# Kernel optimization log

Measured on AMD Instinct MI355X. Metric: run time of the kernel, lower is better.

The kernel has to match this reference:

```python
import jax, jax.numpy as jnp
import numpy as np

EPS = 1.1920929e-07  # torch.finfo(float32).eps
TOP_K = 2
AUX_COEF = 0.01

def rmsnorm(x):
    return x * jax.lax.rsqrt(jnp.mean(x * x, axis=-1, keepdims=True) + EPS)

def setup_inputs() -> dict:
    key = jax.random.key(0)
    ks = jax.random.split(key, 8)
    B, T, C, H, E = 1, 2048, 1024, 2048, 8
    x = jax.random.normal(ks[0], (B, T, C), jnp.float32)
    gate_w = jax.random.normal(ks[1], (E, C), jnp.float32) * 0.02
    w1 = jax.random.normal(ks[2], (E, H, C), jnp.float32) * 0.02  # expert up-proj
    w2 = jax.random.normal(ks[3], (E, C, H), jnp.float32) * 0.02  # expert down-proj
    shared_gate_w = jax.random.normal(ks[4], (1, C), jnp.float32) * 0.02
    k_w = jax.random.normal(ks[5], (H, C), jnp.float32) * 0.02
    k_b = jax.random.normal(ks[6], (H,), jnp.float32) * 0.01
    v_w = jax.random.normal(ks[7], (C, H), jnp.float32) * 0.02
    v_b = jnp.zeros((C,), jnp.float32)
    return dict(x=x, gate_w=gate_w, w1=w1, w2=w2, shared_gate_w=shared_gate_w,
                k_w=k_w, k_b=k_b, v_w=v_w, v_b=v_b)

def reference(x, gate_w, w1, w2, shared_gate_w, k_w, k_b, v_w, v_b):
    B, T, C = x.shape
    xt = rmsnorm(x.reshape(-1, C))                     # [N,C]
    N = xt.shape[0]
    raw = xt @ gate_w.T                                # [N,E]
    scores = jax.nn.softmax(raw, axis=-1)
    topk_w, topk_idx = jax.lax.top_k(scores, TOP_K)    # [N,k]
    topk_w = topk_w / (jnp.sum(topk_w, axis=-1, keepdims=True) + 1e-6)
    E = scores.shape[-1]
    rows = jnp.arange(N)[:, None]
    onehot = jnp.zeros_like(scores).at[rows, topk_idx].set(1.0 / TOP_K)
    aux_loss = E * jnp.sum(jnp.mean(onehot, 0) * jnp.mean(scores, 0)) * AUX_COEF
    # dense gate matrix [N,E]: combine weight per (token, expert)
    g = jnp.zeros_like(scores).at[rows, topk_idx].add(topk_w)
    # grouped-GEMM expressed densely over experts (reference math identical)
    h = jnp.einsum('nc,ehc->neh', xt, w1)              # [N,E,H]
    h = jnp.square(jax.nn.relu(h)) * g[:, :, None]     # act + gate-combine weight
    out = jnp.einsum('neh,ech->nc', h, w2)             # [N,C]
    # shared expert: sigmoid gate * MLP (MLP re-norms its input)
    sg = jax.nn.sigmoid(xt @ shared_gate_w.T)          # [N,1]
    xs = rmsnorm(xt)
    kk = jnp.square(jax.nn.relu(xs @ k_w.T + k_b))     # [N,H]
    shared = kk @ v_w.T + v_b                          # [N,C]
    out = out + sg * shared
    return out.reshape(B, T, C), aux_loss
```

## Files before the change

kernel.cpp:

```cpp
#include <hip/hip_runtime.h>
#include <hip/hip_bf16.h>
#include <stdint.h>

typedef __bf16 bf16;
typedef bf16 bf16x8 __attribute__((ext_vector_type(8)));
typedef bf16 bf16x4 __attribute__((ext_vector_type(4)));
typedef float f32x4 __attribute__((ext_vector_type(4)));

constexpr int N = 2048;
constexpr int C = 1024;
constexpr int H = 2048;
constexpr int E = 8;
constexpr float EPS = 1.1920929e-07f;

constexpr int BM = 128, BN = 256, BK = 32;
constexpr int GT = 32;
constexpr int ATILE = BM * BK * 2;
constexpr int BTILE = BN * BK * 2;

constexpr int PREP_GATE = N / GT;
constexpr int PREP_RMS  = N;
constexpr int CVT_BLK   = ((E * H * C + H * C) / 4) / 1024;
constexpr int PREP_TOTAL = PREP_GATE + PREP_RMS + 2 * CVT_BLK;

constexpr int P1_UP    = E * (N / BM) * (H / BN);
constexpr int P1_KP    = (N / BM) * (H / BN);
constexpr int P1_TOTAL = P1_UP + P1_KP;

constexpr int P2_DOWN  = (E * 2) * (N / BM) * (C / BN);
constexpr int P2_VP    = (N / BM) * (C / BN) * 2;
constexpr int P2_TOTAL = P2_DOWN + P2_VP;

constexpr int COMBINE_BLK = (N * C / 4) / 256;

__device__ __forceinline__ void cvt_pair(const float* __restrict__ s1, bf16* __restrict__ d1,
                                         size_t n1, const float* __restrict__ s2,
                                         bf16* __restrict__ d2, int cbx) {
  size_t base = (size_t)cbx * 1024 + threadIdx.x;
  #pragma unroll
  for (int j = 0; j < 4; ++j) {
    size_t i = base + (size_t)j * 256;
    if (i < n1) {
      float4 v = ((const float4*)s1)[i];
      bf16x4 o = { (bf16)v.x, (bf16)v.y, (bf16)v.z, (bf16)v.w };
      ((bf16x4*)d1)[i] = o;
    } else {
      size_t k = i - n1;
      float4 v = ((const float4*)s2)[k];
      bf16x4 o = { (bf16)v.x, (bf16)v.y, (bf16)v.z, (bf16)v.w };
      ((bf16x4*)d2)[k] = o;
    }
  }
}

__global__ __launch_bounds__(256) void prep_kernel(
    const float* __restrict__ x, const float* __restrict__ gate_w,
    const float* __restrict__ sgw, const float* __restrict__ w1,
    const float* __restrict__ kw, const float* __restrict__ w2,
    const float* __restrict__ vw,
    bf16* __restrict__ xtb, float* __restrict__ rs2_arr,
    float* __restrict__ g, float* __restrict__ sgbuf,
    int* __restrict__ counts, int* __restrict__ lists,
    float* __restrict__ scoresums,
    bf16* __restrict__ w1b, bf16* __restrict__ kwb,
    bf16* __restrict__ w2b, bf16* __restrict__ vwb) {
  __shared__ float s_scores[8];
  __shared__ int   s_cnt[8];
  __shared__ int   s_base[8];
  __shared__ int   s_e1[GT], s_p1[GT], s_e2[GT], s_p2[GT];
  __shared__ float red[4];
  __shared__ float tot;
  const int bx = blockIdx.x;
  const int tid = threadIdx.x, lane = tid & 63, wave = tid >> 6;

  if (bx >= PREP_GATE + PREP_RMS + CVT_BLK) {
    cvt_pair(w2, w2b, (size_t)E * C * H / 4, vw, vwb,
             bx - PREP_GATE - PREP_RMS - CVT_BLK);
    return;
  }
  if (bx >= PREP_GATE + PREP_RMS) {
    cvt_pair(w1, w1b, (size_t)E * H * C / 4, kw, kwb, bx - PREP_GATE - PREP_RMS);
    return;
  }
  if (bx >= PREP_GATE) {
    int n = bx - PREP_GATE;
    float4 v = ((const float4*)(x + (size_t)n * C))[tid];
    float ss = v.x*v.x + v.y*v.y + v.z*v.z + v.w*v.w;
    #pragma unroll
    for (int off = 32; off > 0; off >>= 1) ss += __shfl_down(ss, off, 64);
    if (lane == 0) red[wave] = ss;
    __syncthreads();
    if (tid == 0) tot = red[0] + red[1] + red[2] + red[3];
    __syncthreads();
    float sumsq = tot;
    float rs1 = rsqrtf(sumsq * (1.f / C) + EPS);
    bf16x4 o = { (bf16)(v.x*rs1), (bf16)(v.y*rs1), (bf16)(v.z*rs1), (bf16)(v.w*rs1) };
    ((bf16x4*)(xtb + (size_t)n * C))[tid] = o;
    if (tid == 0) {
      float m2 = sumsq * rs1 * rs1 * (1.f / C);
      rs2_arr[n] = rsqrtf(m2 + EPS);
    }
    return;
  }
  if (tid < 8) { s_scores[tid] = 0.f; s_cnt[tid] = 0; }
  __syncthreads();

  const int tok0 = bx * GT + wave * (GT / 4);
  for (int tt = 0; tt < GT / 4; ++tt) {
    const int tok = tok0 + tt;
    const float* xr = x + (size_t)tok * C;
    float acc[10];
    #pragma unroll
    for (int e = 0; e < 10; e++) acc[e] = 0.f;
    #pragma unroll
    for (int k = 0; k < 16; ++k) {
      int c = k * 64 + lane;
      float xv = xr[c];
      #pragma unroll
      for (int e = 0; e < 8; e++) acc[e] = fmaf(xv, gate_w[e * 1024 + c], acc[e]);
      acc[8] = fmaf(xv, sgw[c], acc[8]);
      acc[9] = fmaf(xv, xv, acc[9]);
    }
    #pragma unroll
    for (int e = 0; e < 10; e++) {
      float v = acc[e];
      #pragma unroll
      for (int off = 32; off > 0; off >>= 1) v += __shfl_xor(v, off, 64);
      acc[e] = v;
    }
    if (lane == 0) {
      float rs1 = rsqrtf(acc[9] * (1.f / C) + EPS);
      float raw[9];
      #pragma unroll
      for (int e = 0; e < 9; e++) raw[e] = acc[e] * rs1;
      float m = raw[0];
      for (int e = 1; e < 8; e++) m = fmaxf(m, raw[e]);
      float sc[8], s = 0.f;
      for (int e = 0; e < 8; e++) { sc[e] = expf(raw[e] - m); s += sc[e]; }
      float inv = 1.f / s;
      for (int e = 0; e < 8; e++) sc[e] *= inv;
      int i1 = 0;
      for (int e = 1; e < 8; e++) if (sc[e] > sc[i1]) i1 = e;
      int i2 = -1;
      for (int e = 0; e < 8; e++) {
        if (e == i1) continue;
        if (i2 < 0 || sc[e] > sc[i2]) i2 = e;
      }
      float denom = sc[i1] + sc[i2] + 1e-6f;
      float* gr = g + (size_t)tok * E;
      #pragma unroll
      for (int e = 0; e < 8; e++) gr[e] = 0.f;
      gr[i1] = sc[i1] / denom;
      gr[i2] = sc[i2] / denom;
      sgbuf[tok] = 1.f / (1.f + expf(-raw[8]));
      for (int e = 0; e < 8; e++) atomicAdd(&s_scores[e], sc[e]);
      int lt = wave * (GT / 4) + tt;
      int p1 = atomicAdd(&s_cnt[i1], 1);
      int p2 = atomicAdd(&s_cnt[i2], 1);
      s_e1[lt] = i1; s_p1[lt] = p1;
      s_e2[lt] = i2; s_p2[lt] = p2;
    }
  }
  __syncthreads();
  if (tid < 8) {
    s_base[tid] = atomicAdd(&counts[tid], s_cnt[tid]);
    atomicAdd(&scoresums[tid], s_scores[tid]);
  }
  __syncthreads();
  if (tid < GT) {
    int tok = bx * GT + tid;
    int e1 = s_e1[tid], e2 = s_e2[tid];
    lists[e1 * N + s_base[e1] + s_p1[tid]] = (tok << 1);
    lists[e2 * N + s_base[e2] + s_p2[tid]] = (tok << 1) | 1;
  }
}

#define GLL(gp, lp)                                                             \
  __builtin_amdgcn_global_load_lds((__attribute__((address_space(1))) void*)(gp), \
                                   (__attribute__((address_space(3))) void*)(lp), 16, 0, 0)

__device__ __forceinline__ void stage_step(
    const char* pA, const char* pB0, const char* pB1,
    char* Ab, char* Bb, int dA, int dB) {
  GLL(pA, Ab + dA);
  GLL(pB0, Bb + dB);
  GLL(pB1, Bb + dB + 1024);
}

__device__ __forceinline__ void mfma_loop(
    const char* pA, const char* pB0, const char* pB1,
    char* As, char* Bs, int dA, int dB, int lane,
    int kIters, int mb, int nb, f32x4 acc[4][4]) {
  const int arow = lane & 15;
  const int koff = (lane >> 4) * 16;
  stage_step(pA, pB0, pB1, As, Bs, dA, dB);
  pA += 64; pB0 += 64; pB1 += 64;
  for (int t = 0; t < kIters; ++t) {
    if (t + 1 < kIters) {
      stage_step(pA, pB0, pB1,
                 As + ((t + 1) & 1) * ATILE, Bs + ((t + 1) & 1) * BTILE, dA, dB);
      pA += 64; pB0 += 64; pB1 += 64;
      asm volatile("s_waitcnt vmcnt(3)" ::: "memory");
    } else {
      asm volatile("s_waitcnt vmcnt(0)" ::: "memory");
    }
    __builtin_amdgcn_s_barrier();
    const char* Ac = As + (t & 1) * ATILE;
    const char* Bc = Bs + (t & 1) * BTILE;
    bf16x8 a[4], b[4];
    #pragma unroll
    for (int i = 0; i < 4; ++i) {
      a[i] = *(const bf16x8*)(Ac + (mb + i * 16 + arow) * 64 + koff);
      b[i] = *(const bf16x8*)(Bc + (nb + i * 16 + arow) * 64 + koff);
    }
    #pragma unroll
    for (int i = 0; i < 4; ++i)
      #pragma unroll
      for (int j = 0; j < 4; ++j)
        acc[i][j] = __builtin_amdgcn_mfma_f32_16x16x32_bf16(a[i], b[j], acc[i][j], 0, 0, 0);
    __builtin_amdgcn_s_barrier();
  }
}

#define GEMM_VARS                                                  \
  const int tid = threadIdx.x;                                     \
  const int lane = tid & 63, wave = tid >> 6;            \
  const int mb = (wave >> 2) * 64, nb = (wave & 3) * 64;           \
  const int sra = wave * 16 + (lane >> 2);      \
  const int srb = wave * 32 + (lane >> 2);      \
  const int scb = (lane & 3) * 16;             \
  const int dA = wave * 1024, dB = wave * 2048;                    \
  const int col = lane & 15, quad = lane >> 4;                     \
  f32x4 acc[4][4] = {};

__device__ __forceinline__ void run_up(
    const bf16* __restrict__ xtb, const bf16* __restrict__ w1b,
    const float* __restrict__ g, const int* __restrict__ lists,
    const int* __restrict__ counts, bf16* __restrict__ hb,
    int e, int m0, int h0, char* As, char* Bs, int* toks) {
  const int cnt = counts[e];
  if (m0 >= cnt) return;
  GEMM_VARS
  if (tid < BM) toks[tid] = lists[e * N + min(m0 + tid, cnt - 1)];
  __syncthreads();
  const char* pA  = (const char*)xtb + ((size_t)(toks[sra] >> 1) * C) * 2 + scb;
  const char* pB0 = (const char*)w1b + ((size_t)e * H * C + (size_t)(h0 + srb) * C) * 2 + scb;
  const char* pB1 = pB0 + (size_t)16 * C * 2;
  mfma_loop(pA, pB0, pB1, As, Bs, dA, dB, lane, C / BK, mb, nb, acc);
  #pragma unroll
  for (int mi = 0; mi < 4; mi++) {
    #pragma unroll
    for (int r = 0; r < 4; r++) {
      int ml = mb + mi * 16 + quad * 4 + r;
      if (m0 + ml < cnt) {
        int packed = toks[ml];
        float gv = g[(size_t)(packed >> 1) * E + e];
        size_t base = (size_t)packed * H + h0 + nb;
        #pragma unroll
        for (int ni = 0; ni < 4; ni++) {
          float v = fmaxf(acc[mi][ni][r], 0.f);
          hb[base + ni * 16 + col] = (bf16)(v * v * gv);
        }
      }
    }
  }
}

__device__ __forceinline__ void run_kproj(
    const bf16* __restrict__ xtb, const bf16* __restrict__ kwb,
    const float* __restrict__ rs2, const float* __restrict__ k_b,
    bf16* __restrict__ kkb, int n0, int h0, char* As, char* Bs) {
  GEMM_VARS
  const char* pA  = (const char*)xtb + ((size_t)(n0 + sra) * C) * 2 + scb;
  const char* pB0 = (const char*)kwb + ((size_t)(h0 + srb) * C) * 2 + scb;
  const char* pB1 = pB0 + (size_t)16 * C * 2;
  mfma_loop(pA, pB0, pB1, As, Bs, dA, dB, lane, C / BK, mb, nb, acc);
  #pragma unroll
  for (int mi = 0; mi < 4; mi++) {
    #pragma unroll
    for (int r = 0; r < 4; r++) {
      int n = n0 + mb + mi * 16 + quad * 4 + r;
      float rs = rs2[n];
      #pragma unroll
      for (int ni = 0; ni < 4; ni++) {
        int h = h0 + nb + ni * 16 + col;
        float v = fmaf(acc[mi][ni][r], rs, k_b[h]);
        v = fmaxf(v, 0.f);
        kkb[(size_t)n * H + h] = (bf16)(v * v);
      }
    }
  }
}

__device__ __forceinline__ void run_down(
    const bf16* __restrict__ hb, const bf16* __restrict__ w2b,
    const int* __restrict__ lists, const int* __restrict__ counts,
    float* __restrict__ dp, int e, int ks, int m0, int c0,
    char* As, char* Bs, int* toks) {
  const int cnt = counts[e];
  if (m0 >= cnt) return;
  GEMM_VARS
  if (tid < BM) toks[tid] = lists[e * N + min(m0 + tid, cnt - 1)];
  __syncthreads();
  const size_t kofs = (size_t)ks * (H / 2) * 2;
  const char* pA  = (const char*)hb + ((size_t)toks[sra] * H) * 2 + kofs + scb;
  const char* pB0 = (const char*)w2b + ((size_t)e * C * H + (size_t)(c0 + srb) * H) * 2 + kofs + scb;
  const char* pB1 = pB0 + (size_t)16 * H * 2;
  mfma_loop(pA, pB0, pB1, As, Bs, dA, dB, lane, (H / 2) / BK, mb, nb, acc);
  #pragma unroll
  for (int mi = 0; mi < 4; mi++) {
    #pragma unroll
    for (int r = 0; r < 4; r++) {
      int ml = mb + mi * 16 + quad * 4 + r;
      if (m0 + ml < cnt) {
        int packed = toks[ml];
        int tok = packed >> 1, par = packed & 1;
        float* orow = dp + (((size_t)(ks * 2 + par) * N + tok) * C) + c0 + nb;
        #pragma unroll
        for (int ni = 0; ni < 4; ni++) orow[ni * 16 + col] = acc[mi][ni][r];
      }
    }
  }
}

__device__ __forceinline__ void run_vproj(
    const bf16* __restrict__ kkb, const bf16* __restrict__ vwb,
    float* __restrict__ vp, int n0, int c0, int ks, char* As, char* Bs) {
  GEMM_VARS
  const size_t kofs = (size_t)ks * (H / 2) * 2;
  const char* pA  = (const char*)kkb + ((size_t)(n0 + sra) * H) * 2 + kofs + scb;
  const char* pB0 = (const char*)vwb + ((size_t)(c0 + srb) * H) * 2 + kofs + scb;
  const char* pB1 = pB0 + (size_t)16 * H * 2;
  mfma_loop(pA, pB0, pB1, As, Bs, dA, dB, lane, (H / 2) / BK, mb, nb, acc);
  #pragma unroll
  for (int mi = 0; mi < 4; mi++) {
    #pragma unroll
    for (int r = 0; r < 4; r++) {
      int n = n0 + mb + mi * 16 + quad * 4 + r;
      float* orow = vp + ((size_t)ks * N + n) * C + c0 + nb;
      #pragma unroll
      for (int ni = 0; ni < 4; ni++) orow[ni * 16 + col] = acc[mi][ni][r];
    }
  }
}

__global__ __launch_bounds__(512) void phase1_kernel(
    const bf16* __restrict__ xtb, const bf16* __restrict__ w1b,
    const float* __restrict__ g, const int* __restrict__ lists,
    const int* __restrict__ counts, bf16* __restrict__ hb,
    const bf16* __restrict__ kwb, const float* __restrict__ rs2,
    const float* __restrict__ k_b, bf16* __restrict__ kkb) {
  __shared__ __align__(16) char As[2 * ATILE];
  __shared__ __align__(16) char Bs[2 * BTILE];
  __shared__ int toks[BM];
  const int bx = blockIdx.x;
  if (bx < P1_UP) {
    int e = bx >> 7, rem = bx & 127;
    int h0 = (rem & 7) * BN, m0 = (rem >> 3) * BM;
    run_up(xtb, w1b, g, lists, counts, hb, e, m0, h0, As, Bs, toks);
  } else {
    int rem = bx - P1_UP;
    int n0 = (rem & 15) * BM, h0 = (rem >> 4) * BN;
    run_kproj(xtb, kwb, rs2, k_b, kkb, n0, h0, As, Bs);
  }
}

__global__ __launch_bounds__(512) void phase2_kernel(
    const bf16* __restrict__ hb, const bf16* __restrict__ w2b,
    const int* __restrict__ lists, const int* __restrict__ counts,
    const bf16* __restrict__ kkb, const bf16* __restrict__ vwb,
    float* __restrict__ dp, float* __restrict__ vp) {
  __shared__ __align__(16) char As[2 * ATILE];
  __shared__ __align__(16) char Bs[2 * BTILE];
  __shared__ int toks[BM];
  const int bx = blockIdx.x;
  if (bx < P2_DOWN) {
    int z = bx >> 6, rem = bx & 63;
    int e = z >> 1, ks = z & 1;
    int c0 = (rem & 3) * BN, m0 = (rem >> 2) * BM;
    run_down(hb, w2b, lists, counts, dp, e, ks, m0, c0, As, Bs, toks);
  } else {
    int rem = bx - P2_DOWN;
    int ks = rem >> 6, r2 = rem & 63;
    int n0 = (r2 & 15) * BM, c0 = (r2 >> 4) * BN;
    run_vproj(kkb, vwb, vp, n0, c0, ks, As, Bs);
  }
}

__global__ __launch_bounds__(256) void combine_kernel(
    const float* __restrict__ dp, const float* __restrict__ vp,
    const float* __restrict__ v_b, const float* __restrict__ sg,
    const float* __restrict__ scoresums, const int* __restrict__ counts,
    float* __restrict__ out) {
  constexpr size_t NC = (size_t)N * C;
  if (blockIdx.x == 0 && threadIdx.x == 0) {
    float a = 0.f;
    for (int e = 0; e < 8; e++)
      a += (0.5f * (float)counts[e] * (1.f / N)) * (scoresums[e] * (1.f / N));
    out[NC] = 8.f * a * 0.01f;
  }
  size_t i = (size_t)blockIdx.x * 256 + threadIdx.x;
  size_t off = i * 4;
  int n = (int)(off >> 10);
  int c = (int)(off & 1023);
  float4 a = ((const float4*)(dp))[i];
  float4 b = ((const float4*)(dp + NC))[i];
  float4 d2 = ((const float4*)(dp + 2 * NC))[i];
  float4 d3 = ((const float4*)(dp + 3 * NC))[i];
  float4 u = ((const float4*)(vp))[i];
  float4 w = ((const float4*)(vp + NC))[i];
  float4 bias = *(const float4*)(v_b + c);
  float s = sg[n];
  float4 o;
  o.x = a.x + b.x + d2.x + d3.x + s * (u.x + w.x + bias.x);
  o.y = a.y + b.y + d2.y + d3.y + s * (u.y + w.y + bias.y);
  o.z = a.z + b.z + d2.z + d3.z + s * (u.z + w.z + bias.z);
  o.w = a.w + b.w + d2.w + d3.w + s * (u.w + w.w + bias.w);
  ((float4*)out)[i] = o;
}

extern "C" void kernel_launch(void* const* d_in, const int* in_sizes, int n_in,
                              void* d_out, int out_size, void* d_ws, size_t ws_size,
                              hipStream_t stream) {
  (void)in_sizes; (void)n_in; (void)ws_size; (void)out_size;
  const float* x   = (const float*)d_in[0];
  const float* gw  = (const float*)d_in[1];
  const float* w1  = (const float*)d_in[2];
  const float* w2  = (const float*)d_in[3];
  const float* sgw = (const float*)d_in[4];
  const float* k_w = (const float*)d_in[5];
  const float* k_b = (const float*)d_in[6];
  const float* v_w = (const float*)d_in[7];
  const float* v_b = (const float*)d_in[8];
  float* out = (float*)d_out;

  char* p = (char*)d_ws;
  auto alloc = [&](size_t bytes) { char* r = p; p += (bytes + 255) & ~255ull; return r; };
  bf16* xtb  = (bf16*)alloc((size_t)N * C * 2);
  bf16* w1b  = (bf16*)alloc((size_t)E * H * C * 2);
  bf16* w2b  = (bf16*)alloc((size_t)E * C * H * 2);
  bf16* kwb  = (bf16*)alloc((size_t)H * C * 2);
  bf16* vwb  = (bf16*)alloc((size_t)C * H * 2);
  bf16* hb   = (bf16*)alloc((size_t)2 * N * H * 2);
  bf16* kkb  = (bf16*)alloc((size_t)N * H * 2);
  float* rs2 = (float*)alloc((size_t)N * 4);
  float* g   = (float*)alloc((size_t)N * E * 4);
  float* sg  = (float*)alloc((size_t)N * 4);
  float* scoresums = (float*)alloc(256);
  int* counts = (int*)alloc(256);
  int* lists  = (int*)alloc((size_t)E * N * 4);
  float* vp   = (float*)alloc((size_t)2 * N * C * 4);
  float* dp   = (float*)w1b;

  hipMemsetAsync(scoresums, 0, 512, stream);
  prep_kernel<<<PREP_TOTAL, 256, 0, stream>>>(
      x, gw, sgw, w1, k_w, w2, v_w, xtb, rs2, g, sg, counts, lists, scoresums,
      w1b, kwb, w2b, vwb);
  phase1_kernel<<<P1_TOTAL, 512, 0, stream>>>(
      xtb, w1b, g, lists, counts, hb, kwb, rs2, k_b, kkb);
  phase2_kernel<<<P2_TOTAL, 512, 0, stream>>>(
      hb, w2b, lists, counts, kkb, vwb, dp, vp);
  combine_kernel<<<COMBINE_BLK, 256, 0, stream>>>(
      dp, vp, v_b, sg, scoresums, counts, out);
}
```

Before: 299.2 us.

## Merge all phases into one persistent kernel with atomic work queues and grid barriers

Replaces the four separate launches (prep, up/kproj, down/vproj, combine) with one persistent kernel of 256 blocks by 512 threads. Each block pulls work items from per-phase atomic counters, and software grid barriers separate the phases. The w2/v_w bf16 conversion moves into phase 1 so it overlaps the up-projection GEMMs. The GEMM inner loop drops its LDS double buffering for a single buffer with two full syncs per k-step. That risks exposing load latency, with only one block resident per CU to hide it.

```diff
diff --git a/kernel.cpp b/kernel.cpp
--- a/kernel.cpp
+++ b/kernel.cpp
@@ -13,33 +13,45 @@
 constexpr int E = 8;
 constexpr float EPS = 1.1920929e-07f;
 
+constexpr int NBLK = 256;
+constexpr int NTHR = 512;
 constexpr int BM = 128, BN = 256, BK = 32;
 constexpr int GT = 32;
-constexpr int ATILE = BM * BK * 2;
-constexpr int BTILE = BN * BK * 2;
-
-constexpr int PREP_GATE = N / GT;
-constexpr int PREP_RMS  = N;
-constexpr int CVT_BLK   = ((E * H * C + H * C) / 4) / 1024;
-constexpr int PREP_TOTAL = PREP_GATE + PREP_RMS + 2 * CVT_BLK;
-
-constexpr int P1_UP    = E * (N / BM) * (H / BN);
-constexpr int P1_KP    = (N / BM) * (H / BN);
-constexpr int P1_TOTAL = P1_UP + P1_KP;
-
-constexpr int P2_DOWN  = (E * 2) * (N / BM) * (C / BN);
-constexpr int P2_VP    = (N / BM) * (C / BN) * 2;
-constexpr int P2_TOTAL = P2_DOWN + P2_VP;
-
-constexpr int COMBINE_BLK = (N * C / 4) / 256;
-
-__device__ __forceinline__ void cvt_pair(const float* __restrict__ s1, bf16* __restrict__ d1,
-                                         size_t n1, const float* __restrict__ s2,
-                                         bf16* __restrict__ d2, int cbx) {
-  size_t base = (size_t)cbx * 1024 + threadIdx.x;
-  #pragma unroll
-  for (int j = 0; j < 4; ++j) {
-    size_t i = base + (size_t)j * 256;
+
+constexpr int G_GATE = N / GT;
+constexpr int G_RMS  = N / 8;
+constexpr int CVT_F4 = (E * H * C + H * C) / 4;
+constexpr int CVT_ITEMS = CVT_F4 / 4096;
+constexpr int P0_ITEMS = G_GATE + G_RMS + CVT_ITEMS;
+
+constexpr int P1_UP = E * (N / BM) * (H / BN);
+constexpr int P1_KP = (N / BM) * (H / BN);
+constexpr int P1_ITEMS = P1_UP + P1_KP + CVT_ITEMS;
+
+constexpr int P2_DOWN = (E * 2) * (N / BM) * (C / BN);
+constexpr int P2_VP = (N / BM) * (C / BN) * 2;
+constexpr int P2_ITEMS = P2_DOWN + P2_VP;
+
+constexpr int P3_ITEMS = (N * C / 4) / 2048;
+
+__device__ __forceinline__ void grid_barrier(int* bar, int tid) {
+  __syncthreads();
+  __threadfence();
+  if (tid == 0) {
+    atomicAdd(bar, 1);
+    while (atomicAdd(bar, 0) < NBLK) __builtin_amdgcn_s_sleep(8);
+  }
+  __syncthreads();
+  __threadfence();
+}
+
+__device__ __forceinline__ void cvt8(const float* __restrict__ s1, bf16* __restrict__ d1,
+                                     size_t n1, const float* __restrict__ s2,
+                                     bf16* __restrict__ d2, int item) {
+  size_t base = (size_t)item * 4096 + threadIdx.x;
+  #pragma unroll
+  for (int j = 0; j < 8; ++j) {
+    size_t i = base + (size_t)j * 512;
     if (i < n1) {
       float4 v = ((const float4*)s1)[i];
       bf16x4 o = { (bf16)v.x, (bf16)v.y, (bf16)v.z, (bf16)v.w };
@@ -53,60 +65,47 @@
   }
 }
 
-__global__ __launch_bounds__(256) void prep_kernel(
-    const float* __restrict__ x, const float* __restrict__ gate_w,
-    const float* __restrict__ sgw, const float* __restrict__ w1,
-    const float* __restrict__ kw, const float* __restrict__ w2,
-    const float* __restrict__ vw,
-    bf16* __restrict__ xtb, float* __restrict__ rs2_arr,
-    float* __restrict__ g, float* __restrict__ sgbuf,
-    int* __restrict__ counts, int* __restrict__ lists,
-    float* __restrict__ scoresums,
-    bf16* __restrict__ w1b, bf16* __restrict__ kwb,
-    bf16* __restrict__ w2b, bf16* __restrict__ vwb) {
-  __shared__ float s_scores[8];
-  __shared__ int   s_cnt[8];
-  __shared__ int   s_base[8];
-  __shared__ int   s_e1[GT], s_p1[GT], s_e2[GT], s_p2[GT];
-  __shared__ float red[4];
-  __shared__ float tot;
-  const int bx = blockIdx.x;
+__device__ __forceinline__ void rms_item(int it, const float* __restrict__ x,
+                                         bf16* __restrict__ xtb,
+                                         float* __restrict__ rs2_arr) {
+  const int lane = threadIdx.x & 63, wave = threadIdx.x >> 6;
+  const int n = it * 8 + wave;
+  const float4* xr = (const float4*)(x + (size_t)n * C);
+  float4 v[4];
+  float ss = 0.f;
+  #pragma unroll
+  for (int j = 0; j < 4; ++j) {
+    v[j] = xr[j * 64 + lane];
+    ss += v[j].x * v[j].x + v[j].y * v[j].y + v[j].z * v[j].z + v[j].w * v[j].w;
+  }
+  #pragma unroll
+  for (int off = 32; off > 0; off >>= 1) ss += __shfl_xor(ss, off, 64);
+  float rs1 = rsqrtf(ss * (1.f / C) + EPS);
+  bf16x4* ot = (bf16x4*)(xtb + (size_t)n * C);
+  #pragma unroll
+  for (int j = 0; j < 4; ++j) {
+    bf16x4 o = { (bf16)(v[j].x * rs1), (bf16)(v[j].y * rs1),
+                 (bf16)(v[j].z * rs1), (bf16)(v[j].w * rs1) };
+    ot[j * 64 + lane] = o;
+  }
+  if (lane == 0) {
+    float m2 = ss * rs1 * rs1 * (1.f / C);
+    rs2_arr[n] = rsqrtf(m2 + EPS);
+  }
+}
+
+__device__ __forceinline__ void gate_item(
+    int it, const float* __restrict__ x, const float* __restrict__ gate_w,
+    const float* __restrict__ sgw, float* __restrict__ g,
+    float* __restrict__ sgbuf, int* __restrict__ counts,
+    int* __restrict__ lists, float* __restrict__ scoresums,
+    float* s_scores, int* s_cnt, int* s_base,
+    int* s_e1, int* s_p1, int* s_e2, int* s_p2) {
   const int tid = threadIdx.x, lane = tid & 63, wave = tid >> 6;
-
-  if (bx >= PREP_GATE + PREP_RMS + CVT_BLK) {
-    cvt_pair(w2, w2b, (size_t)E * C * H / 4, vw, vwb,
-             bx - PREP_GATE - PREP_RMS - CVT_BLK);
-    return;
-  }
-  if (bx >= PREP_GATE + PREP_RMS) {
-    cvt_pair(w1, w1b, (size_t)E * H * C / 4, kw, kwb, bx - PREP_GATE - PREP_RMS);
-    return;
-  }
-  if (bx >= PREP_GATE) {
-    int n = bx - PREP_GATE;
-    float4 v = ((const float4*)(x + (size_t)n * C))[tid];
-    float ss = v.x*v.x + v.y*v.y + v.z*v.z + v.w*v.w;
-    #pragma unroll
-    for (int off = 32; off > 0; off >>= 1) ss += __shfl_down(ss, off, 64);
-    if (lane == 0) red[wave] = ss;
-    __syncthreads();
-    if (tid == 0) tot = red[0] + red[1] + red[2] + red[3];
-    __syncthreads();
-    float sumsq = tot;
-    float rs1 = rsqrtf(sumsq * (1.f / C) + EPS);
-    bf16x4 o = { (bf16)(v.x*rs1), (bf16)(v.y*rs1), (bf16)(v.z*rs1), (bf16)(v.w*rs1) };
-    ((bf16x4*)(xtb + (size_t)n * C))[tid] = o;
-    if (tid == 0) {
-      float m2 = sumsq * rs1 * rs1 * (1.f / C);
-      rs2_arr[n] = rsqrtf(m2 + EPS);
-    }
-    return;
-  }
   if (tid < 8) { s_scores[tid] = 0.f; s_cnt[tid] = 0; }
   __syncthreads();
-
-  const int tok0 = bx * GT + wave * (GT / 4);
-  for (int tt = 0; tt < GT / 4; ++tt) {
+  const int tok0 = it * GT + wave * 4;
+  for (int tt = 0; tt < 4; ++tt) {
     const int tok = tok0 + tt;
     const float* xr = x + (size_t)tok * C;
     float acc[10];
@@ -154,7 +153,7 @@
       gr[i2] = sc[i2] / denom;
       sgbuf[tok] = 1.f / (1.f + expf(-raw[8]));
       for (int e = 0; e < 8; e++) atomicAdd(&s_scores[e], sc[e]);
-      int lt = wave * (GT / 4) + tt;
+      int lt = wave * 4 + tt;
       int p1 = atomicAdd(&s_cnt[i1], 1);
       int p2 = atomicAdd(&s_cnt[i2], 1);
       s_e1[lt] = i1; s_p1[lt] = p1;
@@ -168,7 +167,7 @@
   }
   __syncthreads();
   if (tid < GT) {
-    int tok = bx * GT + tid;
+    int tok = it * GT + tid;
     int e1 = s_e1[tid], e2 = s_e2[tid];
     lists[e1 * N + s_base[e1] + s_p1[tid]] = (tok << 1);
     lists[e2 * N + s_base[e2] + s_p2[tid]] = (tok << 1) | 1;
@@ -178,14 +177,6 @@
 #define GLL(gp, lp)                                                             \
   __builtin_amdgcn_global_load_lds((__attribute__((address_space(1))) void*)(gp), \
                                    (__attribute__((address_space(3))) void*)(lp), 16, 0, 0)
-
-__device__ __forceinline__ void stage_step(
-    const char* pA, const char* pB0, const char* pB1,
-    char* Ab, char* Bb, int dA, int dB) {
-  GLL(pA, Ab + dA);
-  GLL(pB0, Bb + dB);
-  GLL(pB1, Bb + dB + 1024);
-}
 
 __device__ __forceinline__ void mfma_loop(
     const char* pA, const char* pB0, const char* pB1,
@@ -193,32 +184,24 @@
     int kIters, int mb, int nb, f32x4 acc[4][4]) {
   const int arow = lane & 15;
   const int koff = (lane >> 4) * 16;
-  stage_step(pA, pB0, pB1, As, Bs, dA, dB);
-  pA += 64; pB0 += 64; pB1 += 64;
-  for (int t = 0; t < kIters; ++t) {
-    if (t + 1 < kIters) {
-      stage_step(pA, pB0, pB1,
-                 As + ((t + 1) & 1) * ATILE, Bs + ((t + 1) & 1) * BTILE, dA, dB);
-      pA += 64; pB0 += 64; pB1 += 64;
-      asm volatile("s_waitcnt vmcnt(3)" ::: "memory");
-    } else {
-      asm volatile("s_waitcnt vmcnt(0)" ::: "memory");
-    }
-    __builtin_amdgcn_s_barrier();
-    const char* Ac = As + (t & 1) * ATILE;
-    const char* Bc = Bs + (t & 1) * BTILE;
+  for (int kt = 0; kt < kIters; ++kt) {
+    GLL(pA, As + dA);
+    GLL(pB0, Bs + dB);
+    GLL(pB1, Bs + dB + 1024);
+    pA += BK * 2; pB0 += BK * 2; pB1 += BK * 2;
+    __syncthreads();
     bf16x8 a[4], b[4];
     #pragma unroll
     for (int i = 0; i < 4; ++i) {
-      a[i] = *(const bf16x8*)(Ac + (mb + i * 16 + arow) * 64 + koff);
-      b[i] = *(const bf16x8*)(Bc + (nb + i * 16 + arow) * 64 + koff);
+      a[i] = *(const bf16x8*)(As + (mb + i * 16 + arow) * 64 + koff);
+      b[i] = *(const bf16x8*)(Bs + (nb + i * 16 + arow) * 64 + koff);
     }
     #pragma unroll
     for (int i = 0; i < 4; ++i)
       #pragma unroll
       for (int j = 0; j < 4; ++j)
         acc[i][j] = __builtin_amdgcn_mfma_f32_16x16x32_bf16(a[i], b[j], acc[i][j], 0, 0, 0);
-    __builtin_amdgcn_s_barrier();
+    __syncthreads();
   }
 }
 
@@ -344,79 +327,132 @@
   }
 }
 
-__global__ __launch_bounds__(512) void phase1_kernel(
-    const bf16* __restrict__ xtb, const bf16* __restrict__ w1b,
-    const float* __restrict__ g, const int* __restrict__ lists,
-    const int* __restrict__ counts, bf16* __restrict__ hb,
-    const bf16* __restrict__ kwb, const float* __restrict__ rs2,
-    const float* __restrict__ k_b, bf16* __restrict__ kkb) {
-  __shared__ __align__(16) char As[2 * ATILE];
-  __shared__ __align__(16) char Bs[2 * BTILE];
-  __shared__ int toks[BM];
-  const int bx = blockIdx.x;
-  if (bx < P1_UP) {
-    int e = bx >> 7, rem = bx & 127;
-    int h0 = (rem & 7) * BN, m0 = (rem >> 3) * BM;
-    run_up(xtb, w1b, g, lists, counts, hb, e, m0, h0, As, Bs, toks);
-  } else {
-    int rem = bx - P1_UP;
-    int n0 = (rem & 15) * BM, h0 = (rem >> 4) * BN;
-    run_kproj(xtb, kwb, rs2, k_b, kkb, n0, h0, As, Bs);
-  }
-}
-
-__global__ __launch_bounds__(512) void phase2_kernel(
-    const bf16* __restrict__ hb, const bf16* __restrict__ w2b,
-    const int* __restrict__ lists, const int* __restrict__ counts,
-    const bf16* __restrict__ kkb, const bf16* __restrict__ vwb,
-    float* __restrict__ dp, float* __restrict__ vp) {
-  __shared__ __align__(16) char As[2 * ATILE];
-  __shared__ __align__(16) char Bs[2 * BTILE];
-  __shared__ int toks[BM];
-  const int bx = blockIdx.x;
-  if (bx < P2_DOWN) {
-    int z = bx >> 6, rem = bx & 63;
-    int e = z >> 1, ks = z & 1;
-    int c0 = (rem & 3) * BN, m0 = (rem >> 2) * BM;
-    run_down(hb, w2b, lists, counts, dp, e, ks, m0, c0, As, Bs, toks);
-  } else {
-    int rem = bx - P2_DOWN;
-    int ks = rem >> 6, r2 = rem & 63;
-    int n0 = (r2 & 15) * BM, c0 = (r2 >> 4) * BN;
-    run_vproj(kkb, vwb, vp, n0, c0, ks, As, Bs);
-  }
-}
-
-__global__ __launch_bounds__(256) void combine_kernel(
-    const float* __restrict__ dp, const float* __restrict__ vp,
+__device__ __forceinline__ void combine_item(
+    int it, const float* __restrict__ dp, const float* __restrict__ vp,
     const float* __restrict__ v_b, const float* __restrict__ sg,
     const float* __restrict__ scoresums, const int* __restrict__ counts,
     float* __restrict__ out) {
   constexpr size_t NC = (size_t)N * C;
-  if (blockIdx.x == 0 && threadIdx.x == 0) {
+  if (it == 0 && threadIdx.x == 0) {
     float a = 0.f;
     for (int e = 0; e < 8; e++)
       a += (0.5f * (float)counts[e] * (1.f / N)) * (scoresums[e] * (1.f / N));
     out[NC] = 8.f * a * 0.01f;
   }
-  size_t i = (size_t)blockIdx.x * 256 + threadIdx.x;
-  size_t off = i * 4;
-  int n = (int)(off >> 10);
-  int c = (int)(off & 1023);
-  float4 a = ((const float4*)(dp))[i];
-  float4 b = ((const float4*)(dp + NC))[i];
-  float4 d2 = ((const float4*)(dp + 2 * NC))[i];
-  float4 d3 = ((const float4*)(dp + 3 * NC))[i];
-  float4 u = ((const float4*)(vp))[i];
-  float4 w = ((const float4*)(vp + NC))[i];
-  float4 bias = *(const float4*)(v_b + c);
-  float s = sg[n];
-  float4 o;
-  o.x = a.x + b.x + d2.x + d3.x + s * (u.x + w.x + bias.x);
-  o.y = a.y + b.y + d2.y + d3.y + s * (u.y + w.y + bias.y);
-  o.z = a.z + b.z + d2.z + d3.z + s * (u.z + w.z + bias.z);
-  o.w = a.w + b.w + d2.w + d3.w + s * (u.w + w.w + bias.w);
-  ((float4*)out)[i] = o;
+  size_t base = (size_t)it * 2048 + threadIdx.x;
+  #pragma unroll
+  for (int j = 0; j < 4; ++j) {
+    size_t i = base + (size_t)j * 512;
+    size_t off = i * 4;
+    int n = (int)(off >> 10);
+    int c = (int)(off & 1023);
+    float4 a = ((const float4*)(dp))[i];
+    float4 b = ((const float4*)(dp + NC))[i];
+    float4 d2 = ((const float4*)(dp + 2 * NC))[i];
+    float4 d3 = ((const float4*)(dp + 3 * NC))[i];
+    float4 u = ((const float4*)(vp))[i];
+    float4 w = ((const float4*)(vp + NC))[i];
+    float4 bias = *(const float4*)(v_b + c);
+    float s = sg[n];
+    float4 o;
+    o.x = a.x + b.x + d2.x + d3.x + s * (u.x + w.x + bias.x);
+    o.y = a.y + b.y + d2.y + d3.y + s * (u.y + w.y + bias.y);
+    o.z = a.z + b.z + d2.z + d3.z + s * (u.z + w.z + bias.z);
+    o.w = a.w + b.w + d2.w + d3.w + s * (u.w + w.w + bias.w);
+    ((float4*)out)[i] = o;
+  }
+}
+
+__global__ __launch_bounds__(NTHR) void mega_kernel(
+    const float* __restrict__ x, const float* __restrict__ gate_w,
+    const float* __restrict__ sgw, const float* __restrict__ w1,
+    const float* __restrict__ kw, const float* __restrict__ w2,
+    const float* __restrict__ vw, const float* __restrict__ k_b,
+    const float* __restrict__ v_b,
+    bf16* __restrict__ xtb, float* __restrict__ rs2,
+    float* __restrict__ g, float* __restrict__ sg,
+    int* __restrict__ counts, int* __restrict__ lists,
+    float* __restrict__ scoresums,
+    bf16* __restrict__ w1b, bf16* __restrict__ kwb,
+    bf16* __restrict__ w2b, bf16* __restrict__ vwb,
+    bf16* __restrict__ hb, bf16* __restrict__ kkb,
+    float* __restrict__ dp, float* __restrict__ vp,
+    float* __restrict__ out, int* __restrict__ qc) {
+  __shared__ __align__(16) char As[BM * BK * 2];
+  __shared__ __align__(16) char Bs[BN * BK * 2];
+  __shared__ int toks[BM];
+  __shared__ float s_scores[8];
+  __shared__ int s_cnt[8], s_base[8];
+  __shared__ int s_e1[GT], s_p1[GT], s_e2[GT], s_p2[GT];
+  __shared__ int s_item;
+  const int tid = threadIdx.x;
+  int* bar = qc + 32;
+
+  for (;;) {
+    __syncthreads();
+    if (tid == 0) s_item = atomicAdd(&qc[0], 1);
+    __syncthreads();
+    int it = s_item;
+    if (it >= P0_ITEMS) break;
+    if (it < G_GATE) {
+      gate_item(it, x, gate_w, sgw, g, sg, counts, lists, scoresums,
+                s_scores, s_cnt, s_base, s_e1, s_p1, s_e2, s_p2);
+    } else if (it < G_GATE + G_RMS) {
+      rms_item(it - G_GATE, x, xtb, rs2);
+    } else {
+      cvt8(w1, w1b, (size_t)E * H * C / 4, kw, kwb, it - G_GATE - G_RMS);
+    }
+  }
+  grid_barrier(&bar[0], tid);
+
+  for (;;) {
+    __syncthreads();
+    if (tid == 0) s_item = atomicAdd(&qc[1], 1);
+    __syncthreads();
+    int it = s_item;
+    if (it >= P1_ITEMS) break;
+    if (it < P1_UP) {
+      int e = it >> 7, rem = it & 127;
+      int h0 = (rem & 7) * BN, m0 = (rem >> 3) * BM;
+      run_up(xtb, w1b, g, lists, counts, hb, e, m0, h0, As, Bs, toks);
+    } else if (it < P1_UP + P1_KP) {
+      int rem = it - P1_UP;
+      int n0 = (rem & 15) * BM, h0 = (rem >> 4) * BN;
+      run_kproj(xtb, kwb, rs2, k_b, kkb, n0, h0, As, Bs);
+    } else {
+      cvt8(w2, w2b, (size_t)E * C * H / 4, vw, vwb, it - P1_UP - P1_KP);
+    }
+  }
+  grid_barrier(&bar[1], tid);
+
+  for (;;) {
+    __syncthreads();
+    if (tid == 0) s_item = atomicAdd(&qc[2], 1);
+    __syncthreads();
+    int it = s_item;
+    if (it >= P2_ITEMS) break;
+    if (it < P2_DOWN) {
+      int z = it >> 6, rem = it & 63;
+      int e = z >> 1, ks = z & 1;
+      int c0 = (rem & 3) * BN, m0 = (rem >> 2) * BM;
+      run_down(hb, w2b, lists, counts, dp, e, ks, m0, c0, As, Bs, toks);
+    } else {
+      int rem = it - P2_DOWN;
+      int ks = rem >> 6, r2 = rem & 63;
+      int n0 = (r2 & 15) * BM, c0 = (r2 >> 4) * BN;
+      run_vproj(kkb, vwb, vp, n0, c0, ks, As, Bs);
+    }
+  }
+  grid_barrier(&bar[2], tid);
+
+  for (;;) {
+    __syncthreads();
+    if (tid == 0) s_item = atomicAdd(&qc[3], 1);
+    __syncthreads();
+    int it = s_item;
+    if (it >= P3_ITEMS) break;
+    combine_item(it, dp, vp, v_b, sg, scoresums, counts, out);
+  }
 }
 
 extern "C" void kernel_launch(void* const* d_in, const int* in_sizes, int n_in,
@@ -448,18 +484,14 @@
   float* sg  = (float*)alloc((size_t)N * 4);
   float* scoresums = (float*)alloc(256);
   int* counts = (int*)alloc(256);
+  int* qc     = (int*)alloc(256);
   int* lists  = (int*)alloc((size_t)E * N * 4);
   float* vp   = (float*)alloc((size_t)2 * N * C * 4);
   float* dp   = (float*)w1b;
 
-  hipMemsetAsync(scoresums, 0, 512, stream);
-  prep_kernel<<<PREP_TOTAL, 256, 0, stream>>>(
-      x, gw, sgw, w1, k_w, w2, v_w, xtb, rs2, g, sg, counts, lists, scoresums,
-      w1b, kwb, w2b, vwb);
-  phase1_kernel<<<P1_TOTAL, 512, 0, stream>>>(
-      xtb, w1b, g, lists, counts, hb, kwb, rs2, k_b, kkb);
-  phase2_kernel<<<P2_TOTAL, 512, 0, stream>>>(
-      hb, w2b, lists, counts, kkb, vwb, dp, vp);
-  combine_kernel<<<COMBINE_BLK, 256, 0, stream>>>(
-      dp, vp, v_b, sg, scoresums, counts, out);
-}
+  hipMemsetAsync(scoresums, 0, 768, stream);
+  mega_kernel<<<NBLK, NTHR, 0, stream>>>(
+      x, gw, sgw, w1, k_w, w2, v_w, k_b, v_b,
+      xtb, rs2, g, sg, counts, lists, scoresums,
+      w1b, kwb, w2b, vwb, hb, kkb, dp, vp, out, qc);
+}
```

Measured after the change: 630.9 us. 111% more time.
